# Optimization experiments

Measured on AMD Instinct MI355X. Metric: run time of the kernel, lower is better.

## Reference

```python
import jax, jax.numpy as jnp
import numpy as np

N_NODES = 50000
N_EDGES = 800000
F_IN, F_HID, F_OUT = 128, 256, 256


def setup_inputs() -> dict:
    key = jax.random.key(0)
    ks = jax.random.split(key, 8)
    x = jax.random.normal(ks[0], (N_NODES, F_IN), dtype=jnp.float32)
    edge_index = jax.random.randint(ks[1], (2, N_EDGES), 0, N_NODES, dtype=jnp.int64)

    def lin(k, fan_in, fan_out):
        return jax.random.normal(k, (fan_in, fan_out), dtype=jnp.float32) / np.sqrt(fan_in).astype(np.float32)

    return {
        "x": x,
        "edge_index": edge_index,
        "W1": lin(ks[2], F_IN, F_HID),  "b1": jnp.zeros((F_HID,), jnp.float32),
        "W2": lin(ks[3], F_HID, F_HID), "b2": jnp.zeros((F_HID,), jnp.float32),
        "W3": lin(ks[4], F_HID, F_OUT), "b3": jnp.zeros((F_OUT,), jnp.float32),
    }


def reference(x, edge_index, W1, b1, W2, b2, W3, b3):
    # GCN (eval mode): edge_drop and feature dropout are identity; bn=False.
    n = x.shape[0]
    loops = jnp.arange(n, dtype=edge_index.dtype)
    src = jnp.concatenate([edge_index[0], loops])  # [E+N] with self-loops
    dst = jnp.concatenate([edge_index[1], loops])

    # Symmetric normalization deg^{-1/2}[src] * deg^{-1/2}[dst] (deg over dst incl. self-loops)
    deg = jax.ops.segment_sum(jnp.ones_like(dst, dtype=x.dtype), dst, num_segments=n)
    dinv = jnp.where(deg > 0, jax.lax.rsqrt(deg), jnp.zeros_like(deg))
    norm = dinv[src] * dinv[dst]  # [E+N]

    def gcn_conv(h, W, b):
        h = h @ W                                       # [N, out]
        msg = h[src] * norm[:, None]                    # gather + scale  [E+N, out]
        return jax.ops.segment_sum(msg, dst, num_segments=n) + b  # scatter-add

    h = jax.nn.relu(gcn_conv(x, W1, b1))
    h = jax.nn.relu(gcn_conv(h, W2, b2))
    return gcn_conv(h, W3, b3)
```

## Files before the change

### kernel.cpp

```cpp
#include <hip/hip_runtime.h>
#include <hip/hip_bf16.h>

#define NNODES 50000
#define NEDGES 800000
#define F_IN 128
#define F_HID 256

using u16 = unsigned short;
using u32 = unsigned int;
using f32x4 = __attribute__((ext_vector_type(4))) float;
using s16x8 = __attribute__((ext_vector_type(8))) short;

constexpr int B2SHIFT = 9;
constexpr int NB2 = (NNODES + 511) >> 9;
constexpr int NBLK = 256;
constexpr int EPB = NEDGES / NBLK;

constexpr size_t OFF_DINV   = 0;
constexpr size_t OFF_ROWPTR = 200192;
constexpr size_t OFF_CMAT   = 400384;
constexpr size_t OFF_BTOT   = 500736;
constexpr size_t OFF_BBASE  = 501760;
constexpr size_t OFF_PAIRS  = 502784;
constexpr size_t OFF_PW     = 3702784;
constexpr size_t OFF_XB     = 6902784;
constexpr size_t OFF_HB     = 19702784;
constexpr size_t OFF_AGGB   = 45302784;
constexpr size_t OFF_W1T    = 70902784;
constexpr size_t OFF_W2T    = 70968320;
constexpr size_t OFF_W3T    = 71099392;

static __device__ __forceinline__ float b2f(u16 u) {
    union { unsigned int i; float f; } v;
    v.i = ((unsigned int)u) << 16;
    return v.f;
}
static __device__ __forceinline__ u16 f2b(float f) {
    __hip_bfloat16 h = __float2bfloat16(f);
    return __builtin_bit_cast(u16, h);
}

static __device__ __forceinline__ bool detect_wide(const void* raw) {
    __shared__ int bad;
    if (threadIdx.x == 0) bad = 0;
    __syncthreads();
    unsigned long long v = ((const unsigned long long*)raw)[threadIdx.x & 255];
    if (v >= (unsigned long long)NNODES) atomicAdd(&bad, 1);
    __syncthreads();
    return bad == 0;
}

__global__ __launch_bounds__(256) void hist_kernel(const void* __restrict__ raw, int* __restrict__ cmat) {
    const bool wide = detect_wide(raw);
    __shared__ int h[NB2];
    int t = threadIdx.x;
    if (t < NB2) h[t] = 0;
    __syncthreads();
    const int base = blockIdx.x * EPB;
    for (int i = t; i < EPB; i += 256) {
        int e = base + i;
        int d = wide ? (int)((const long long*)raw)[NEDGES + e] : ((const int*)raw)[NEDGES + e];
        atomicAdd(&h[d >> B2SHIFT], 1);
    }
    __syncthreads();
    if (t < NB2) cmat[t * NBLK + blockIdx.x] = h[t];
}

__global__ __launch_bounds__(256) void offset_kernel(int* __restrict__ cmat, int* __restrict__ btot) {
    __shared__ int s[256];
    int b = blockIdx.x;
    int t = threadIdx.x;
    int v = cmat[b * NBLK + t];
    s[t] = v;
    __syncthreads();
    for (int o = 1; o < 256; o <<= 1) {
        int tmp = (t >= o) ? s[t - o] : 0;
        __syncthreads();
        s[t] += tmp;
        __syncthreads();
    }
    cmat[b * NBLK + t] = s[t] - v;
    if (t == 255) btot[b] = s[255];
}

__global__ void bscan_kernel(const int* __restrict__ btot, int* __restrict__ bbase) {
    __shared__ int s[128];
    int t = threadIdx.x;
    int v = (t < NB2) ? btot[t] : 0;
    s[t] = v;
    __syncthreads();
    for (int o = 1; o < 128; o <<= 1) {
        int tmp = (t >= o) ? s[t - o] : 0;
        __syncthreads();
        s[t] += tmp;
        __syncthreads();
    }
    if (t < NB2) bbase[t] = s[t] - v;
}

__global__ __launch_bounds__(256) void scatter_kernel(const void* __restrict__ raw,
                                                      const int* __restrict__ cmat,
                                                      const int* __restrict__ bbase,
                                                      u32* __restrict__ pairs) {
    const bool wide = detect_wide(raw);
    __shared__ int cur[NB2];
    int t = threadIdx.x;
    if (t < NB2) cur[t] = cmat[t * NBLK + blockIdx.x] + bbase[t];
    __syncthreads();
    const int base = blockIdx.x * EPB;
    for (int i = t; i < EPB; i += 256) {
        int e = base + i;
        int s, d;
        if (wide) {
            const long long* p = (const long long*)raw;
            s = (int)p[e];
            d = (int)p[NEDGES + e];
        } else {
            const int* p = (const int*)raw;
            s = p[e];
            d = p[NEDGES + e];
        }
        int pos = atomicAdd(&cur[d >> B2SHIFT], 1);
        pairs[pos] = ((u32)(d & 511) << 16) | (u32)s;
    }
}

__global__ __launch_bounds__(256) void phase2a(const u32* __restrict__ pairs,
                                               const int* __restrict__ bbase, const int* __restrict__ btot,
                                               int* __restrict__ row_ptr, float* __restrict__ dinv) {
    __shared__ int lcnt[512];
    __shared__ int ssc[512];
    int b = blockIdx.x, t = threadIdx.x;
    int n0 = b << B2SHIFT;
    lcnt[t] = 0; lcnt[t + 256] = 0;
    __syncthreads();
    int p0 = bbase[b], p1 = p0 + btot[b];
    for (int p = p0 + t; p < p1; p += 256)
        atomicAdd(&lcnt[pairs[p] >> 16], 1);
    __syncthreads();
    int c0 = lcnt[t], c1 = lcnt[t + 256];
    ssc[t] = c0; ssc[t + 256] = c1;
    __syncthreads();
    for (int o = 1; o < 512; o <<= 1) {
        int a0 = (t >= o) ? ssc[t - o] : 0;
        int a1 = ssc[t + 256 - o];
        __syncthreads();
        ssc[t] += a0; ssc[t + 256] += a1;
        __syncthreads();
    }
    int na = n0 + t, nb = n0 + t + 256;
    if (na < NNODES) { row_ptr[na] = p0 + ssc[t] - c0;       dinv[na] = rsqrtf((float)c0 + 1.0f); }
    if (nb < NNODES) { row_ptr[nb] = p0 + ssc[t + 256] - c1; dinv[nb] = rsqrtf((float)c1 + 1.0f); }
    if (b == 0 && t == 0) row_ptr[NNODES] = NEDGES;
}

__global__ __launch_bounds__(256) void phase2b(const u32* __restrict__ pairs,
                                               const int* __restrict__ bbase, const int* __restrict__ btot,
                                               const int* __restrict__ row_ptr, const float* __restrict__ dinv,
                                               u32* __restrict__ pw) {
    __shared__ int lcur[512];
    int b = blockIdx.x, t = threadIdx.x;
    int n0 = b << B2SHIFT;
    int na = n0 + t, nb = n0 + t + 256;
    lcur[t]       = (na < NNODES) ? row_ptr[na] : NEDGES;
    lcur[t + 256] = (nb < NNODES) ? row_ptr[nb] : NEDGES;
    __syncthreads();
    int p0 = bbase[b], p1 = p0 + btot[b];
    for (int p = p0 + t; p < p1; p += 256) {
        u32 pk = pairs[p];
        int dl = (int)(pk >> 16);
        int src = (int)(pk & 0xFFFFu);
        int pos = atomicAdd(&lcur[dl], 1);
        pw[pos] = ((u32)f2b(dinv[src]) << 16) | (u32)src;
    }
}

__global__ __launch_bounds__(256) void convert_all(const float* __restrict__ x,
                                                   const float* __restrict__ W1, const float* __restrict__ W2,
                                                   const float* __restrict__ W3, u16* __restrict__ xb,
                                                   u16* __restrict__ W1t, u16* __restrict__ W2t,
                                                   u16* __restrict__ W3t) {
    int bid = blockIdx.x;
    if (bid < 6250) {
        int i = bid * 256 + threadIdx.x;
        float4 v = ((const float4*)x)[i];
        ushort4 o;
        o.x = f2b(v.x); o.y = f2b(v.y); o.z = f2b(v.z); o.w = f2b(v.w);
        ((ushort4*)xb)[i] = o;
    } else {
        int idx = (bid - 6250) * 256 + threadIdx.x;
        if (idx < 32768) {
            int k = idx >> 8, n = idx & 255;
            W1t[n * 128 + k] = f2b(W1[idx]);
        } else if (idx < 98304) {
            int j = idx - 32768;
            int k = j >> 8, n = j & 255;
            W2t[n * 256 + k] = f2b(W2[j]);
        } else {
            int j = idx - 98304;
            int k = j >> 8, n = j & 255;
            W3t[n * 256 + k] = f2b(W3[j]);
        }
    }
}

template <int F>
__global__ __launch_bounds__(256) void agg_kernel(const u16* __restrict__ h,
                                                  const int* __restrict__ row_ptr,
                                                  const u32* __restrict__ pw,
                                                  const float* __restrict__ dinv,
                                                  u16* __restrict__ outb) {
    constexpr int VEC = F / 64;
    int lane = threadIdx.x & 63;
    int v = __builtin_amdgcn_readfirstlane((int)(blockIdx.x * 4 + (threadIdx.x >> 6)));
    const size_t lo = (size_t)lane * VEC;

    const int e0 = row_ptr[v], e1 = row_ptr[v + 1];
    float dv = dinv[v];
    float acc[VEC];
    {
        const u16* p = h + (size_t)v * F + lo;
        if constexpr (VEC == 4) {
            ushort4 t = *(const ushort4*)p;
            acc[0] = dv * b2f(t.x); acc[1] = dv * b2f(t.y); acc[2] = dv * b2f(t.z); acc[3] = dv * b2f(t.w);
        } else {
            ushort2 t = *(const ushort2*)p;
            acc[0] = dv * b2f(t.x); acc[1] = dv * b2f(t.y);
        }
    }
    for (int e = e0; e < e1; e += 16) {
        u32 pk[16];
#pragma unroll
        for (int u = 0; u < 16; ++u) {
            int idx = e + u;
            pk[u] = pw[idx < e1 ? idx : e1 - 1];
        }
        int   c[16];
        float w[16];
#pragma unroll
        for (int u = 0; u < 16; ++u) {
            c[u] = (int)(pk[u] & 0xFFFFu);
            w[u] = (e + u < e1) ? b2f((u16)(pk[u] >> 16)) : 0.0f;
        }
        if constexpr (VEC == 4) {
            ushort4 r[16];
#pragma unroll
            for (int u = 0; u < 16; ++u)
                r[u] = *(const ushort4*)(h + (size_t)c[u] * F + lo);
#pragma unroll
            for (int u = 0; u < 16; ++u) {
                acc[0] += w[u] * b2f(r[u].x);
                acc[1] += w[u] * b2f(r[u].y);
                acc[2] += w[u] * b2f(r[u].z);
                acc[3] += w[u] * b2f(r[u].w);
            }
        } else {
            ushort2 r[16];
#pragma unroll
            for (int u = 0; u < 16; ++u)
                r[u] = *(const ushort2*)(h + (size_t)c[u] * F + lo);
#pragma unroll
            for (int u = 0; u < 16; ++u) {
                acc[0] += w[u] * b2f(r[u].x);
                acc[1] += w[u] * b2f(r[u].y);
            }
        }
    }
    u16* o = outb + (size_t)v * F + lo;
    if constexpr (VEC == 4) {
        ushort4 t;
        t.x = f2b(dv * acc[0]); t.y = f2b(dv * acc[1]); t.z = f2b(dv * acc[2]); t.w = f2b(dv * acc[3]);
        *(ushort4*)o = t;
    } else {
        ushort2 t;
        t.x = f2b(dv * acc[0]); t.y = f2b(dv * acc[1]);
        *(ushort2*)o = t;
    }
}

template <int KT, bool RELU, bool OUT_BF16>
__global__ __launch_bounds__(256) void gemm_mfma(const u16* __restrict__ A, const u16* __restrict__ Wt,
                                                 const float* __restrict__ bias, void* __restrict__ outp,
                                                 int M) {
    constexpr int BM = 128, BN = 128, BK = 32;
    __shared__ __align__(16) u16 As[BM * BK];
    __shared__ __align__(16) u16 Bs[BN * BK];
    const int tid = threadIdx.x;
    const int lane = tid & 63, wid = tid >> 6;
    const int l15 = lane & 15, lhi = lane >> 4;
    const int m0 = blockIdx.x * BM, n0 = blockIdx.y * BN;
    const int wr = (wid >> 1) * 64, wc = (wid & 1) * 64;

    f32x4 acc[4][4] = {};

    const int sr = tid >> 1;
    const int sc2 = (tid & 1) * 2;

    for (int k0 = 0; k0 < KT; k0 += BK) {
        uint4 av0, av1, bv0, bv1;
        int ar = m0 + sr;
        if (ar < M) {
            const uint4* ap = (const uint4*)(A + (size_t)ar * KT + k0 + sc2 * 8);
            av0 = ap[0]; av1 = ap[1];
        } else {
            av0 = make_uint4(0, 0, 0, 0); av1 = av0;
        }
        const uint4* bp = (const uint4*)(Wt + (size_t)(n0 + sr) * KT + k0 + sc2 * 8);
        bv0 = bp[0]; bv1 = bp[1];

        __syncthreads();
        *(uint4*)&As[sr * BK + ((sc2 ^ (sr & 3)) * 8)]       = av0;
        *(uint4*)&As[sr * BK + (((sc2 + 1) ^ (sr & 3)) * 8)] = av1;
        *(uint4*)&Bs[sr * BK + ((sc2 ^ (sr & 3)) * 8)]       = bv0;
        *(uint4*)&Bs[sr * BK + (((sc2 + 1) ^ (sr & 3)) * 8)] = bv1;
        __syncthreads();

        s16x8 af[4], bfr[4];
#pragma unroll
        for (int m = 0; m < 4; ++m) {
            int r = wr + m * 16 + l15;
            af[m] = *(const s16x8*)&As[r * BK + ((lhi ^ (r & 3)) * 8)];
        }
#pragma unroll
        for (int n = 0; n < 4; ++n) {
            int r = wc + n * 16 + l15;
            bfr[n] = *(const s16x8*)&Bs[r * BK + ((lhi ^ (r & 3)) * 8)];
        }
#pragma unroll
        for (int m = 0; m < 4; ++m)
#pragma unroll
            for (int n = 0; n < 4; ++n)
                acc[m][n] = __builtin_amdgcn_mfma_f32_16x16x32_bf16(af[m], bfr[n], acc[m][n], 0, 0, 0);
    }

#pragma unroll
    for (int n = 0; n < 4; ++n) {
        int gcol = n0 + wc + n * 16 + l15;
        float bb = bias[gcol];
#pragma unroll
        for (int m = 0; m < 4; ++m) {
            int gr0 = m0 + wr + m * 16 + lhi * 4;
#pragma unroll
            for (int r = 0; r < 4; ++r) {
                int gr = gr0 + r;
                if (gr >= M) continue;
                float vv = acc[m][n][r] + bb;
                if (RELU) vv = vv > 0.f ? vv : 0.f;
                if (OUT_BF16)
                    ((u16*)outp)[(size_t)gr * 256 + gcol] = f2b(vv);
                else
                    ((float*)outp)[(size_t)gr * 256 + gcol] = vv;
            }
        }
    }
}

extern "C" void kernel_launch(void* const* d_in, const int* in_sizes, int n_in,
                              void* d_out, int out_size, void* d_ws, size_t ws_size,
                              hipStream_t stream) {
    const float* x  = (const float*)d_in[0];
    const void* edges = d_in[1];
    const float* W1 = (const float*)d_in[2];
    const float* b1 = (const float*)d_in[3];
    const float* W2 = (const float*)d_in[4];
    const float* b2 = (const float*)d_in[5];
    const float* W3 = (const float*)d_in[6];
    const float* b3 = (const float*)d_in[7];
    float* out = (float*)d_out;

    char* ws = (char*)d_ws;
    float* dinv   = (float*)(ws + OFF_DINV);
    int*   rowptr = (int*)(ws + OFF_ROWPTR);
    int*   cmat   = (int*)(ws + OFF_CMAT);
    int*   btot   = (int*)(ws + OFF_BTOT);
    int*   bbase  = (int*)(ws + OFF_BBASE);
    u32*   pairs  = (u32*)(ws + OFF_PAIRS);
    u32*   pw     = (u32*)(ws + OFF_PW);
    u16*   xb     = (u16*)(ws + OFF_XB);
    u16*   hb     = (u16*)(ws + OFF_HB);
    u16*   aggb   = (u16*)(ws + OFF_AGGB);
    u16*   W1t    = (u16*)(ws + OFF_W1T);
    u16*   W2t    = (u16*)(ws + OFF_W2T);
    u16*   W3t    = (u16*)(ws + OFF_W3T);

    hist_kernel<<<NBLK, 256, 0, stream>>>(edges, cmat);
    offset_kernel<<<NB2, 256, 0, stream>>>(cmat, btot);
    bscan_kernel<<<1, 128, 0, stream>>>(btot, bbase);
    scatter_kernel<<<NBLK, 256, 0, stream>>>(edges, cmat, bbase, pairs);
    phase2a<<<NB2, 256, 0, stream>>>(pairs, bbase, btot, rowptr, dinv);
    phase2b<<<NB2, 256, 0, stream>>>(pairs, bbase, btot, rowptr, dinv, pw);

    convert_all<<<6890, 256, 0, stream>>>(x, W1, W2, W3, xb, W1t, W2t, W3t);

    const int AGG_GRID = NNODES / 4;
    dim3 ggrid((NNODES + 127) / 128, 2);

    agg_kernel<F_IN><<<AGG_GRID, 256, 0, stream>>>(xb, rowptr, pw, dinv, aggb);
    gemm_mfma<F_IN, true, true><<<ggrid, 256, 0, stream>>>(aggb, W1t, b1, hb, NNODES);

    agg_kernel<F_HID><<<AGG_GRID, 256, 0, stream>>>(hb, rowptr, pw, dinv, aggb);
    gemm_mfma<F_HID, true, true><<<ggrid, 256, 0, stream>>>(aggb, W2t, b2, hb, NNODES);

    agg_kernel<F_HID><<<AGG_GRID, 256, 0, stream>>>(hb, rowptr, pw, dinv, aggb);
    gemm_mfma<F_HID, false, false><<<ggrid, 256, 0, stream>>>(aggb, W3t, b3, out, NNODES);
}
```

Baseline: 283.4 us.

## Fuse aggregation with GEMM per layer and merge histogram with conversion

Each GCN layer now aggregates 64 destination rows into shared memory and runs the MFMA GEMM against all 256 output columns in the same block. This removes the intermediate aggregated buffer's global write and read and halves the layer launches. The histogram and the fp32-to-bf16 conversion kernels are merged into one launch. The cost is an 8-edge unroll instead of 16, large shared memory per block (up to 48KB for As), a serial gather phase before the GEMM, and ping-pong hidden buffers.

```diff
diff --git a/kernel.cpp b/kernel.cpp
--- a/kernel.cpp
+++ b/kernel.cpp
@@ -25,7 +25,7 @@
 constexpr size_t OFF_PW     = 3702784;
 constexpr size_t OFF_XB     = 6902784;
 constexpr size_t OFF_HB     = 19702784;
-constexpr size_t OFF_AGGB   = 45302784;
+constexpr size_t OFF_HB2    = 45302784;
 constexpr size_t OFF_W1T    = 70902784;
 constexpr size_t OFF_W2T    = 70968320;
 constexpr size_t OFF_W3T    = 71099392;
@@ -50,26 +50,53 @@
     return bad == 0;
 }
 
-__global__ __launch_bounds__(256) void hist_kernel(const void* __restrict__ raw, int* __restrict__ cmat) {
-    const bool wide = detect_wide(raw);
-    __shared__ int h[NB2];
+__global__ __launch_bounds__(256) void hist_conv(const void* __restrict__ raw, int* __restrict__ cmat,
+                                                 const float* __restrict__ x,
+                                                 const float* __restrict__ W1, const float* __restrict__ W2,
+                                                 const float* __restrict__ W3, u16* __restrict__ xb,
+                                                 u16* __restrict__ W1t, u16* __restrict__ W2t,
+                                                 u16* __restrict__ W3t) {
+    int bid = blockIdx.x;
     int t = threadIdx.x;
-    if (t < NB2) h[t] = 0;
-    __syncthreads();
-    const int base = blockIdx.x * EPB;
-    for (int i = t; i < EPB; i += 256) {
-        int e = base + i;
-        int d = wide ? (int)((const long long*)raw)[NEDGES + e] : ((const int*)raw)[NEDGES + e];
-        atomicAdd(&h[d >> B2SHIFT], 1);
-    }
-    __syncthreads();
-    if (t < NB2) cmat[t * NBLK + blockIdx.x] = h[t];
+    if (bid < NBLK) {
+        const bool wide = detect_wide(raw);
+        __shared__ int h[NB2];
+        if (t < NB2) h[t] = 0;
+        __syncthreads();
+        const int base = bid * EPB;
+        for (int i = t; i < EPB; i += 256) {
+            int e = base + i;
+            int d = wide ? (int)((const long long*)raw)[NEDGES + e] : ((const int*)raw)[NEDGES + e];
+            atomicAdd(&h[d >> B2SHIFT], 1);
+        }
+        __syncthreads();
+        if (t < NB2) cmat[t * NBLK + bid] = h[t];
+    } else if (bid < NBLK + 6250) {
+        int i = (bid - NBLK) * 256 + t;
+        float4 v = ((const float4*)x)[i];
+        ushort4 o;
+        o.x = f2b(v.x); o.y = f2b(v.y); o.z = f2b(v.z); o.w = f2b(v.w);
+        ((ushort4*)xb)[i] = o;
+    } else {
+        int idx = (bid - NBLK - 6250) * 256 + t;
+        if (idx < 32768) {
+            int k = idx >> 8, n = idx & 255;
+            W1t[n * 128 + k] = f2b(W1[idx]);
+        } else if (idx < 98304) {
+            int j = idx - 32768;
+            int k = j >> 8, n = j & 255;
+            W2t[n * 256 + k] = f2b(W2[j]);
+        } else {
+            int j = idx - 98304;
+            int k = j >> 8, n = j & 255;
+            W3t[n * 256 + k] = f2b(W3[j]);
+        }
+    }
 }
 
 __global__ __launch_bounds__(256) void offset_kernel(int* __restrict__ cmat, int* __restrict__ btot) {
     __shared__ int s[256];
-    int b = blockIdx.x;
-    int t = threadIdx.x;
+    int b = blockIdx.x, t = threadIdx.x;
     int v = cmat[b * NBLK + t];
     s[t] = v;
     __syncthreads();
@@ -175,176 +202,129 @@
     }
 }
 
-__global__ __launch_bounds__(256) void convert_all(const float* __restrict__ x,
-                                                   const float* __restrict__ W1, const float* __restrict__ W2,
-                                                   const float* __restrict__ W3, u16* __restrict__ xb,
-                                                   u16* __restrict__ W1t, u16* __restrict__ W2t,
-                                                   u16* __restrict__ W3t) {
-    int bid = blockIdx.x;
-    if (bid < 6250) {
-        int i = bid * 256 + threadIdx.x;
-        float4 v = ((const float4*)x)[i];
-        ushort4 o;
-        o.x = f2b(v.x); o.y = f2b(v.y); o.z = f2b(v.z); o.w = f2b(v.w);
-        ((ushort4*)xb)[i] = o;
-    } else {
-        int idx = (bid - 6250) * 256 + threadIdx.x;
-        if (idx < 32768) {
-            int k = idx >> 8, n = idx & 255;
-            W1t[n * 128 + k] = f2b(W1[idx]);
-        } else if (idx < 98304) {
-            int j = idx - 32768;
-            int k = j >> 8, n = j & 255;
-            W2t[n * 256 + k] = f2b(W2[j]);
+template <int KT, bool RELU, bool OUT_BF16>
+__global__ __launch_bounds__(512, 6) void fused_layer(const u16* __restrict__ h,
+                                                      const int* __restrict__ row_ptr,
+                                                      const u32* __restrict__ pw,
+                                                      const float* __restrict__ dinv,
+                                                      const u16* __restrict__ Wt,
+                                                      const float* __restrict__ bias,
+                                                      void* __restrict__ outp) {
+    constexpr int VEC = KT / 64;
+    constexpr int NK = KT / 32;
+    __shared__ __align__(16) u16 As[64 * KT];
+    __shared__ __align__(16) u16 Bs[256 * 32];
+    const int tid = threadIdx.x;
+    const int lane = tid & 63, w = tid >> 6;
+    const int l15 = lane & 15, lhi = lane >> 4;
+    const int m0 = blockIdx.x * 64;
+
+    for (int i = 0; i < 8; ++i) {
+        const int r = w * 8 + i;
+        const int v = m0 + r;
+        float acc[VEC];
+#pragma unroll
+        for (int q = 0; q < VEC; ++q) acc[q] = 0.f;
+        float dv = 0.f;
+        if (v < NNODES) {
+            const int e0 = row_ptr[v], e1 = row_ptr[v + 1];
+            dv = dinv[v];
+            const u16* sp = h + (size_t)v * KT + lane * VEC;
+            if constexpr (VEC == 4) {
+                ushort4 t = *(const ushort4*)sp;
+                acc[0] = dv * b2f(t.x); acc[1] = dv * b2f(t.y); acc[2] = dv * b2f(t.z); acc[3] = dv * b2f(t.w);
+            } else {
+                ushort2 t = *(const ushort2*)sp;
+                acc[0] = dv * b2f(t.x); acc[1] = dv * b2f(t.y);
+            }
+            for (int e = e0; e < e1; e += 8) {
+                u32 pk[8];
+#pragma unroll
+                for (int u = 0; u < 8; ++u) {
+                    int idx = e + u;
+                    pk[u] = pw[idx < e1 ? idx : e1 - 1];
+                }
+                int   c[8];
+                float wt[8];
+#pragma unroll
+                for (int u = 0; u < 8; ++u) {
+                    c[u] = (int)(pk[u] & 0xFFFFu);
+                    wt[u] = (e + u < e1) ? b2f((u16)(pk[u] >> 16)) : 0.0f;
+                }
+                if constexpr (VEC == 4) {
+                    ushort4 rr[8];
+#pragma unroll
+                    for (int u = 0; u < 8; ++u)
+                        rr[u] = *(const ushort4*)(h + (size_t)c[u] * KT + lane * 4);
+#pragma unroll
+                    for (int u = 0; u < 8; ++u) {
+                        acc[0] += wt[u] * b2f(rr[u].x);
+                        acc[1] += wt[u] * b2f(rr[u].y);
+                        acc[2] += wt[u] * b2f(rr[u].z);
+                        acc[3] += wt[u] * b2f(rr[u].w);
+                    }
+                } else {
+                    ushort2 rr[8];
+#pragma unroll
+                    for (int u = 0; u < 8; ++u)
+                        rr[u] = *(const ushort2*)(h + (size_t)c[u] * KT + lane * 2);
+#pragma unroll
+                    for (int u = 0; u < 8; ++u) {
+                        acc[0] += wt[u] * b2f(rr[u].x);
+                        acc[1] += wt[u] * b2f(rr[u].y);
+                    }
+                }
+            }
+        }
+        if constexpr (VEC == 4) {
+            ushort4 t;
+            t.x = f2b(dv * acc[0]); t.y = f2b(dv * acc[1]); t.z = f2b(dv * acc[2]); t.w = f2b(dv * acc[3]);
+            *(ushort4*)&As[r * KT + (((lane >> 1) ^ (r & 3)) * 8) + (lane & 1) * 4] = t;
         } else {
-            int j = idx - 98304;
-            int k = j >> 8, n = j & 255;
-            W3t[n * 256 + k] = f2b(W3[j]);
-        }
-    }
-}
-
-template <int F>
-__global__ __launch_bounds__(256) void agg_kernel(const u16* __restrict__ h,
-                                                  const int* __restrict__ row_ptr,
-                                                  const u32* __restrict__ pw,
-                                                  const float* __restrict__ dinv,
-                                                  u16* __restrict__ outb) {
-    constexpr int VEC = F / 64;
-    int lane = threadIdx.x & 63;
-    int v = __builtin_amdgcn_readfirstlane((int)(blockIdx.x * 4 + (threadIdx.x >> 6)));
-    const size_t lo = (size_t)lane * VEC;
-
-    const int e0 = row_ptr[v], e1 = row_ptr[v + 1];
-    float dv = dinv[v];
-    float acc[VEC];
-    {
-        const u16* p = h + (size_t)v * F + lo;
-        if constexpr (VEC == 4) {
-            ushort4 t = *(const ushort4*)p;
-            acc[0] = dv * b2f(t.x); acc[1] = dv * b2f(t.y); acc[2] = dv * b2f(t.z); acc[3] = dv * b2f(t.w);
-        } else {
-            ushort2 t = *(const ushort2*)p;
-            acc[0] = dv * b2f(t.x); acc[1] = dv * b2f(t.y);
-        }
-    }
-    for (int e = e0; e < e1; e += 16) {
-        u32 pk[16];
-#pragma unroll
-        for (int u = 0; u < 16; ++u) {
-            int idx = e + u;
-            pk[u] = pw[idx < e1 ? idx : e1 - 1];
-        }
-        int   c[16];
-        float w[16];
-#pragma unroll
-        for (int u = 0; u < 16; ++u) {
-            c[u] = (int)(pk[u] & 0xFFFFu);
-            w[u] = (e + u < e1) ? b2f((u16)(pk[u] >> 16)) : 0.0f;
-        }
-        if constexpr (VEC == 4) {
-            ushort4 r[16];
-#pragma unroll
-            for (int u = 0; u < 16; ++u)
-                r[u] = *(const ushort4*)(h + (size_t)c[u] * F + lo);
-#pragma unroll
-            for (int u = 0; u < 16; ++u) {
-                acc[0] += w[u] * b2f(r[u].x);
-                acc[1] += w[u] * b2f(r[u].y);
-                acc[2] += w[u] * b2f(r[u].z);
-                acc[3] += w[u] * b2f(r[u].w);
-            }
-        } else {
-            ushort2 r[16];
-#pragma unroll
-            for (int u = 0; u < 16; ++u)
-                r[u] = *(const ushort2*)(h + (size_t)c[u] * F + lo);
-#pragma unroll
-            for (int u = 0; u < 16; ++u) {
-                acc[0] += w[u] * b2f(r[u].x);
-                acc[1] += w[u] * b2f(r[u].y);
-            }
-        }
-    }
-    u16* o = outb + (size_t)v * F + lo;
-    if constexpr (VEC == 4) {
-        ushort4 t;
-        t.x = f2b(dv * acc[0]); t.y = f2b(dv * acc[1]); t.z = f2b(dv * acc[2]); t.w = f2b(dv * acc[3]);
-        *(ushort4*)o = t;
-    } else {
-        ushort2 t;
-        t.x = f2b(dv * acc[0]); t.y = f2b(dv * acc[1]);
-        *(ushort2*)o = t;
-    }
-}
-
-template <int KT, bool RELU, bool OUT_BF16>
-__global__ __launch_bounds__(256) void gemm_mfma(const u16* __restrict__ A, const u16* __restrict__ Wt,
-                                                 const float* __restrict__ bias, void* __restrict__ outp,
-                                                 int M) {
-    constexpr int BM = 128, BN = 128, BK = 32;
-    __shared__ __align__(16) u16 As[BM * BK];
-    __shared__ __align__(16) u16 Bs[BN * BK];
-    const int tid = threadIdx.x;
-    const int lane = tid & 63, wid = tid >> 6;
-    const int l15 = lane & 15, lhi = lane >> 4;
-    const int m0 = blockIdx.x * BM, n0 = blockIdx.y * BN;
-    const int wr = (wid >> 1) * 64, wc = (wid & 1) * 64;
-
-    f32x4 acc[4][4] = {};
-
-    const int sr = tid >> 1;
-    const int sc2 = (tid & 1) * 2;
-
-    for (int k0 = 0; k0 < KT; k0 += BK) {
-        uint4 av0, av1, bv0, bv1;
-        int ar = m0 + sr;
-        if (ar < M) {
-            const uint4* ap = (const uint4*)(A + (size_t)ar * KT + k0 + sc2 * 8);
-            av0 = ap[0]; av1 = ap[1];
-        } else {
-            av0 = make_uint4(0, 0, 0, 0); av1 = av0;
-        }
-        const uint4* bp = (const uint4*)(Wt + (size_t)(n0 + sr) * KT + k0 + sc2 * 8);
-        bv0 = bp[0]; bv1 = bp[1];
-
-        __syncthreads();
-        *(uint4*)&As[sr * BK + ((sc2 ^ (sr & 3)) * 8)]       = av0;
-        *(uint4*)&As[sr * BK + (((sc2 + 1) ^ (sr & 3)) * 8)] = av1;
-        *(uint4*)&Bs[sr * BK + ((sc2 ^ (sr & 3)) * 8)]       = bv0;
-        *(uint4*)&Bs[sr * BK + (((sc2 + 1) ^ (sr & 3)) * 8)] = bv1;
-        __syncthreads();
-
-        s16x8 af[4], bfr[4];
+            ushort2 t;
+            t.x = f2b(dv * acc[0]); t.y = f2b(dv * acc[1]);
+            *(ushort2*)&As[r * KT + (((lane >> 2) ^ (r & 3)) * 8) + (lane & 3) * 2] = t;
+        }
+    }
+
+    f32x4 gacc[4][2] = {};
+    const int r2 = tid >> 1, sc2 = (tid & 1) * 2;
+    for (int ks = 0; ks < NK; ++ks) {
+        const int k0 = ks * 32;
+        const uint4* bp = (const uint4*)(Wt + (size_t)r2 * KT + k0 + sc2 * 8);
+        uint4 bv0 = bp[0], bv1 = bp[1];
+        __syncthreads();
+        *(uint4*)&Bs[r2 * 32 + ((sc2 ^ (r2 & 3)) * 8)]       = bv0;
+        *(uint4*)&Bs[r2 * 32 + (((sc2 + 1) ^ (r2 & 3)) * 8)] = bv1;
+        __syncthreads();
+        s16x8 af[4];
 #pragma unroll
         for (int m = 0; m < 4; ++m) {
-            int r = wr + m * 16 + l15;
-            af[m] = *(const s16x8*)&As[r * BK + ((lhi ^ (r & 3)) * 8)];
-        }
-#pragma unroll
-        for (int n = 0; n < 4; ++n) {
-            int r = wc + n * 16 + l15;
-            bfr[n] = *(const s16x8*)&Bs[r * BK + ((lhi ^ (r & 3)) * 8)];
-        }
-#pragma unroll
-        for (int m = 0; m < 4; ++m)
-#pragma unroll
-            for (int n = 0; n < 4; ++n)
-                acc[m][n] = __builtin_amdgcn_mfma_f32_16x16x32_bf16(af[m], bfr[n], acc[m][n], 0, 0, 0);
-    }
-
-#pragma unroll
-    for (int n = 0; n < 4; ++n) {
-        int gcol = n0 + wc + n * 16 + l15;
+            int r = m * 16 + l15;
+            af[m] = *(const s16x8*)&As[r * KT + ((((k0 >> 3) + lhi) ^ (r & 3)) * 8)];
+        }
+#pragma unroll
+        for (int n = 0; n < 2; ++n) {
+            int rb = w * 32 + n * 16 + l15;
+            s16x8 bf_ = *(const s16x8*)&Bs[rb * 32 + ((lhi ^ (rb & 3)) * 8)];
+#pragma unroll
+            for (int m = 0; m < 4; ++m)
+                gacc[m][n] = __builtin_amdgcn_mfma_f32_16x16x32_bf16(af[m], bf_, gacc[m][n], 0, 0, 0);
+        }
+    }
+
+#pragma unroll
+    for (int n = 0; n < 2; ++n) {
+        int gcol = w * 32 + n * 16 + l15;
         float bb = bias[gcol];
 #pragma unroll
         for (int m = 0; m < 4; ++m) {
-            int gr0 = m0 + wr + m * 16 + lhi * 4;
-#pragma unroll
-            for (int r = 0; r < 4; ++r) {
-                int gr = gr0 + r;
-                if (gr >= M) continue;
-                float vv = acc[m][n][r] + bb;
+            int gr0 = m0 + m * 16 + lhi * 4;
+#pragma unroll
+            for (int rr = 0; rr < 4; ++rr) {
+                int gr = gr0 + rr;
+                if (gr >= NNODES) continue;
+                float vv = gacc[m][n][rr] + bb;
                 if (RELU) vv = vv > 0.f ? vv : 0.f;
                 if (OUT_BF16)
                     ((u16*)outp)[(size_t)gr * 256 + gcol] = f2b(vv);
@@ -378,29 +358,21 @@
     u32*   pw     = (u32*)(ws + OFF_PW);
     u16*   xb     = (u16*)(ws + OFF_XB);
     u16*   hb     = (u16*)(ws + OFF_HB);
-    u16*   aggb   = (u16*)(ws + OFF_AGGB);
+    u16*   hb2    = (u16*)(ws + OFF_HB2);
     u16*   W1t    = (u16*)(ws + OFF_W1T);
     u16*   W2t    = (u16*)(ws + OFF_W2T);
     u16*   W3t    = (u16*)(ws + OFF_W3T);
 
-    hist_kernel<<<NBLK, 256, 0, stream>>>(edges, cmat);
+    hist_conv<<<NBLK + 6250 + 640, 256, 0, stream>>>(edges, cmat, x, W1, W2, W3, xb, W1t, W2t, W3t);
     offset_kernel<<<NB2, 256, 0, stream>>>(cmat, btot);
     bscan_kernel<<<1, 128, 0, stream>>>(btot, bbase);
     scatter_kernel<<<NBLK, 256, 0, stream>>>(edges, cmat, bbase, pairs);
     phase2a<<<NB2, 256, 0, stream>>>(pairs, bbase, btot, rowptr, dinv);
     phase2b<<<NB2, 256, 0, stream>>>(pairs, bbase, btot, rowptr, dinv, pw);
 
-    convert_all<<<6890, 256, 0, stream>>>(x, W1, W2, W3, xb, W1t, W2t, W3t);
-
-    const int AGG_GRID = NNODES / 4;
-    dim3 ggrid((NNODES + 127) / 128, 2);
-
-    agg_kernel<F_IN><<<AGG_GRID, 256, 0, stream>>>(xb, rowptr, pw, dinv, aggb);
-    gemm_mfma<F_IN, true, true><<<ggrid, 256, 0, stream>>>(aggb, W1t, b1, hb, NNODES);
-
-    agg_kernel<F_HID><<<AGG_GRID, 256, 0, stream>>>(hb, rowptr, pw, dinv, aggb);
-    gemm_mfma<F_HID, true, true><<<ggrid, 256, 0, stream>>>(aggb, W2t, b2, hb, NNODES);
-
-    agg_kernel<F_HID><<<AGG_GRID, 256, 0, stream>>>(hb, rowptr, pw, dinv, aggb);
-    gemm_mfma<F_HID, false, false><<<ggrid, 256, 0, stream>>>(aggb, W3t, b3, out, NNODES);
-}
+    const int FB = (NNODES + 63) / 64;
+
+    fused_layer<F_IN, true, true><<<FB, 512, 0, stream>>>(xb, rowptr, pw, dinv, W1t, b1, hb);
+    fused_layer<F_HID, true, true><<<FB, 512, 0, stream>>>(hb, rowptr, pw, dinv, W2t, b2, hb2);
+    fused_layer<F_HID, false, false><<<FB, 512, 0, stream>>>(hb2, rowptr, pw, dinv, W3t, b3, out);
+}
```

New measurement: 299.9 us. +5.8%, slower.
